# Kernel tuning notes

Measured on AMD Instinct MI355X. Metric: run time of the kernel, lower is better.

The kernel has to match this reference:

```python
import jax, jax.numpy as jnp
import numpy as np
import math

D_MODEL = 1024
NUM_HEADS = 16
D_K = D_MODEL // NUM_HEADS
THETA = 10000.0
NEG_INF = 1.0e6  # module uses -1e6, not -inf


def _rope_tables(seq_len):
    pair_idx = jnp.arange(0, D_K, 2, dtype=jnp.float32)
    inv_freq = 1.0 / (THETA ** (pair_idx / D_K))
    pos = jnp.arange(seq_len, dtype=jnp.float32)
    angles = jnp.outer(pos, inv_freq)  # (S, D_K//2)
    return jnp.cos(angles), jnp.sin(angles)


def _apply_rope(x, cos, sin):
    # x: (B, H, S, D_K); cos/sin: (S, D_K//2)
    xe = x[..., 0::2]
    xo = x[..., 1::2]
    oe = xe * cos - xo * sin
    oo = xe * sin + xo * cos
    return jnp.stack([oe, oo], axis=-1).reshape(x.shape)


def setup_inputs() -> dict:
    key = jax.random.key(0)
    k0, k1, k2, k3, k4 = jax.random.split(key, 5)
    B, S = 2, 2048
    x = jax.random.normal(k0, (B, S, D_MODEL), dtype=jnp.float32)
    scale = 0.02
    wq = jax.random.normal(k1, (D_MODEL, D_MODEL), dtype=jnp.float32) * scale
    wk = jax.random.normal(k2, (D_MODEL, D_MODEL), dtype=jnp.float32) * scale
    wv = jax.random.normal(k3, (D_MODEL, D_MODEL), dtype=jnp.float32) * scale
    wo = jax.random.normal(k4, (D_MODEL, D_MODEL), dtype=jnp.float32) * scale
    return {"x": x, "wq": wq, "wk": wk, "wv": wv, "wo": wo}


def reference(x, wq, wk, wv, wo):
    B, S, _ = x.shape
    q = x @ wq.T
    k = x @ wk.T
    v = x @ wv.T
    # (B, S, H, d_k) -> (B, H, S, d_k)
    q = q.reshape(B, S, NUM_HEADS, D_K).transpose(0, 2, 1, 3)
    k = k.reshape(B, S, NUM_HEADS, D_K).transpose(0, 2, 1, 3)
    v = v.reshape(B, S, NUM_HEADS, D_K).transpose(0, 2, 1, 3)
    cos, sin = _rope_tables(S)
    q = _apply_rope(q, cos, sin)
    k = _apply_rope(k, cos, sin)
    scores = jnp.einsum("bhqd,bhkd->bhqk", q, k) / math.sqrt(D_K)
    causal = jnp.tril(jnp.ones((S, S), dtype=bool))
    scores = jnp.where(causal, scores, -NEG_INF)
    attn = jax.nn.softmax(scores, axis=-1)
    out = jnp.einsum("bhqk,bhkd->bhqd", attn, v)
    out = out.transpose(0, 2, 1, 3).reshape(B, S, D_MODEL)
    return out @ wo.T
```

## Files before the change

### kernel.cpp

```cpp
#include <hip/hip_runtime.h>

typedef __attribute__((ext_vector_type(8))) __bf16 bf16x8;
typedef __attribute__((ext_vector_type(8))) _Float16 f16x8;
typedef __attribute__((ext_vector_type(4))) float f32x4;
typedef __attribute__((ext_vector_type(8))) unsigned short u16x8;
typedef __attribute__((ext_vector_type(4))) unsigned int u32x4;

#define MFMA_BF16(a, b, c) __builtin_amdgcn_mfma_f32_16x16x32_bf16((a), (b), (c), 0, 0, 0)
#define MFMA_F16(a, b, c)  __builtin_amdgcn_mfma_f32_16x16x32_f16((a), (b), (c), 0, 0, 0)
#define LOG2E 1.44269504088896340736f
#define QSCALE 0.18033688011112042f

__device__ __forceinline__ float b2f(unsigned short u) {
    union { unsigned int i; float f; } v; v.i = ((unsigned int)u) << 16; return v.f;
}
__device__ __forceinline__ unsigned short f2bf(float f) {
    union { float f; unsigned int i; } v; v.f = f;
    unsigned int u = v.i;
    return (unsigned short)((u + 0x7fffu + ((u >> 16) & 1u)) >> 16);
}

__device__ __forceinline__ void gl_lds16(const void* g, void* l) {
    __builtin_amdgcn_global_load_lds(
        (const __attribute__((address_space(1))) void*)g,
        (__attribute__((address_space(3))) void*)l,
        16, 0, 0);
}

__global__ __launch_bounds__(256) void cvt_all(const float* __restrict__ x,
                                               const float* __restrict__ wq,
                                               const float* __restrict__ wk,
                                               const float* __restrict__ wv,
                                               const float* __restrict__ wo,
                                               unsigned short* __restrict__ xb,
                                               unsigned short* __restrict__ wqb,
                                               unsigned short* __restrict__ wkb,
                                               unsigned short* __restrict__ wvb,
                                               unsigned short* __restrict__ wob) {
    int id = blockIdx.x * 256 + threadIdx.x;
    const float* src; unsigned short* dst; size_t off; float scl = 1.0f;
    if (id < 524288)      { src = x;  dst = xb;  off = (size_t)id * 8; }
    else if (id < 655360) { src = wq; dst = wqb; off = (size_t)(id - 524288) * 8; scl = QSCALE; }
    else if (id < 786432) { src = wk; dst = wkb; off = (size_t)(id - 655360) * 8; }
    else if (id < 917504) { src = wv; dst = wvb; off = (size_t)(id - 786432) * 8; }
    else                  { src = wo; dst = wob; off = (size_t)(id - 917504) * 8; }
    float4 a = *(const float4*)(src + off);
    float4 b = *(const float4*)(src + off + 4);
    u16x8 o;
    o[0] = f2bf(a.x * scl); o[1] = f2bf(a.y * scl); o[2] = f2bf(a.z * scl); o[3] = f2bf(a.w * scl);
    o[4] = f2bf(b.x * scl); o[5] = f2bf(b.y * scl); o[6] = f2bf(b.z * scl); o[7] = f2bf(b.w * scl);
    *(u16x8*)(dst + off) = o;
}

template <int MODE>
__device__ __forceinline__ void gemm128_bt(const unsigned short* __restrict__ A,
                                           const unsigned short* __restrict__ B,
                                           void* __restrict__ Cv,
                                           int m0, int n0, int ldc,
                                           unsigned short* As, unsigned short* Bs) {
    const int tid = threadIdx.x;
    const int w = tid >> 6, lane = tid & 63;
    const int quad = lane >> 4, l15 = lane & 15;
    const int wm = w & 1, wn = w >> 1;

    f32x4 acc[4][4];
#pragma unroll
    for (int mt = 0; mt < 4; ++mt)
#pragma unroll
        for (int nt = 0; nt < 4; ++nt) acc[mt][nt] = f32x4{0.f, 0.f, 0.f, 0.f};

    for (int k0 = 0; k0 < 1024; k0 += 32) {
        __syncthreads();
#pragma unroll
        for (int i = 0; i < 2; ++i) {
            int L = (w * 2 + i) * 64 + lane;
            int r = L >> 2;
            int c = (L & 3) ^ ((r >> 1) & 3);
            gl_lds16(A + (size_t)(m0 + r) * 1024 + k0 + c * 8, As + L * 8);
            gl_lds16(B + (size_t)(n0 + r) * 1024 + k0 + c * 8, Bs + L * 8);
        }
        __syncthreads();

        bf16x8 af[4], bfr[4];
#pragma unroll
        for (int mt = 0; mt < 4; ++mt) {
            int row = wm * 64 + mt * 16 + l15;
            af[mt] = *(const bf16x8*)(As + row * 32 + (quad ^ ((row >> 1) & 3)) * 8);
        }
#pragma unroll
        for (int nt = 0; nt < 4; ++nt) {
            int row = wn * 64 + nt * 16 + l15;
            bfr[nt] = *(const bf16x8*)(Bs + row * 32 + (quad ^ ((row >> 1) & 3)) * 8);
        }
#pragma unroll
        for (int mt = 0; mt < 4; ++mt)
#pragma unroll
            for (int nt = 0; nt < 4; ++nt)
                acc[mt][nt] = MFMA_BF16(af[mt], bfr[nt], acc[mt][nt]);
    }

    float invf[4], sgn = 0.f;
    if constexpr (MODE == 3) {
        sgn = (l15 & 1) ? 1.0f : -1.0f;
#pragma unroll
        for (int nt = 0; nt < 4; ++nt)
            invf[nt] = exp2f(-0.41524101186092029f * (float)((nt * 16 + l15) >> 1));
    }

#pragma unroll
    for (int mt = 0; mt < 4; ++mt) {
        int grow = m0 + wm * 64 + mt * 16 + quad * 4;
#pragma unroll
        for (int nt = 0; nt < 4; ++nt) {
            int gcol = n0 + wn * 64 + nt * 16 + l15;
#pragma unroll
            for (int r = 0; r < 4; ++r) {
                float val = acc[mt][nt][r];
                size_t idx = (size_t)(grow + r) * ldc + gcol;
                if constexpr (MODE == 0) {
                    ((unsigned short*)Cv)[idx] = f2bf(val);
                } else if constexpr (MODE == 1) {
                    ((float*)Cv)[idx] = val;
                } else if constexpr (MODE == 2) {
                    _Float16 hv = (_Float16)val;
                    ((unsigned short*)Cv)[idx] = __builtin_bit_cast(unsigned short, hv);
                } else {
                    float p = __shfl_xor(val, 1);
                    float pos = (float)((grow + r) & 2047);
                    float ang = pos * invf[nt];
                    float out = val * __cosf(ang) + sgn * p * __sinf(ang);
                    ((unsigned short*)Cv)[idx] = f2bf(out);
                }
            }
        }
    }
}

__global__ __launch_bounds__(256) void gemm_qkv(const unsigned short* __restrict__ X,
                                                const unsigned short* __restrict__ Wq,
                                                const unsigned short* __restrict__ Wk,
                                                const unsigned short* __restrict__ Wv,
                                                unsigned short* __restrict__ Qo,
                                                unsigned short* __restrict__ Ko,
                                                unsigned short* __restrict__ Vt) {
    __shared__ unsigned short As[128 * 32];
    __shared__ unsigned short Bs[128 * 32];
    int y = blockIdx.y;
    if (y < 16) {
        int sel = y >> 3;
        int m0 = blockIdx.x * 128;
        int n0 = (y & 7) * 128;
        const unsigned short* B = sel ? Wk : Wq;
        unsigned short* C = sel ? Ko : Qo;
        gemm128_bt<3>(X, B, C, m0, n0, 1024, As, Bs);
    } else {
        int m0 = (y & 7) * 128;
        int n0 = blockIdx.x * 128;
        gemm128_bt<2>(Wv, X, Vt, m0, n0, 4096, As, Bs);
    }
}

__global__ __launch_bounds__(256) void gemm_out(const unsigned short* __restrict__ A,
                                                const unsigned short* __restrict__ Wo,
                                                float* __restrict__ C) {
    __shared__ unsigned short As[128 * 32];
    __shared__ unsigned short Bs[128 * 32];
    gemm128_bt<1>(A, Wo, C, blockIdx.x * 128, blockIdx.y * 128, 1024, As, Bs);
}

#define FBODY(KBASE, MASKED)                                                            \
    {                                                                                   \
        bf16x8 kf[4][2];                                                                \
        _Pragma("unroll")                                                               \
        for (int nt = 0; nt < 4; ++nt) {                                                \
            int row = nt * 16 + l15;                                                    \
            const unsigned short* kp = Ksb + row * 64;                                  \
            int swk = row & 7;                                                          \
            kf[nt][0] = *(const bf16x8*)(kp + (quad ^ swk) * 8);                        \
            kf[nt][1] = *(const bf16x8*)(kp + ((quad ^ 4) ^ swk) * 8);                  \
        }                                                                               \
        f16x8 pa[2][2];                                                                 \
        _Pragma("unroll")                                                               \
        for (int mt = 0; mt < 2; ++mt) {                                                \
            f32x4 sc[4];                                                                \
            _Pragma("unroll")                                                           \
            for (int nt = 0; nt < 4; ++nt) {                                            \
                f32x4 z = f32x4{0.f, 0.f, 0.f, 0.f};                                    \
                z = MFMA_BF16(kf[nt][0], qf[mt][0], z);                                 \
                sc[nt] = MFMA_BF16(kf[nt][1], qf[mt][1], z);                            \
            }                                                                           \
            int qpos = qposw + mt * 16 + l15;                                           \
            unsigned pk[8];                                                             \
            _Pragma("unroll")                                                           \
            for (int nt = 0; nt < 4; ++nt) {                                            \
                float e[4];                                                             \
                _Pragma("unroll")                                                       \
                for (int r_ = 0; r_ < 4; ++r_) {                                        \
                    float ev = exp2f(sc[nt][r_]);                                       \
                    if (MASKED) {                                                       \
                        int kpos = (KBASE) + nt * 16 + quad * 4 + r_;                   \
                        ev = (kpos > qpos) ? 0.f : ev;                                  \
                    }                                                                   \
                    e[r_] = ev;                                                         \
                }                                                                       \
                pk[nt * 2 + 0] = __builtin_bit_cast(unsigned,                           \
                                     __builtin_amdgcn_cvt_pkrtz(e[0], e[1]));           \
                pk[nt * 2 + 1] = __builtin_bit_cast(unsigned,                           \
                                     __builtin_amdgcn_cvt_pkrtz(e[2], e[3]));           \
            }                                                                           \
            u32x4 rs0 = u32x4{pk[0], pk[1], pk[2], pk[3]};                              \
            u32x4 rs1 = u32x4{pk[4], pk[5], pk[6], pk[7]};                              \
            lacc[mt] = MFMA_F16(__builtin_bit_cast(f16x8, rs0), ones, lacc[mt]);        \
            lacc[mt] = MFMA_F16(__builtin_bit_cast(f16x8, rs1), ones, lacc[mt]);        \
            int b0 = quad & 1;                                                          \
            unsigned y0 = (unsigned)__builtin_amdgcn_ds_swizzle(                        \
                              (int)(b0 ? pk[0] : pk[2]), 0x401F);                       \
            unsigned y1 = (unsigned)__builtin_amdgcn_ds_swizzle(                        \
                              (int)(b0 ? pk[1] : pk[3]), 0x401F);                       \
            unsigned y2 = (unsigned)__builtin_amdgcn_ds_swizzle(                        \
                              (int)(b0 ? pk[4] : pk[6]), 0x401F);                       \
            unsigned y3 = (unsigned)__builtin_amdgcn_ds_swizzle(                        \
                              (int)(b0 ? pk[5] : pk[7]), 0x401F);                       \
            u32x4 t0 = b0 ? u32x4{y0, y1, pk[2], pk[3]}                                 \
                          : u32x4{pk[0], pk[1], y0, y1};                                \
            u32x4 t1 = b0 ? u32x4{y2, y3, pk[6], pk[7]}                                 \
                          : u32x4{pk[4], pk[5], y2, y3};                                \
            pa[mt][0] = __builtin_bit_cast(f16x8, t0);                                  \
            pa[mt][1] = __builtin_bit_cast(f16x8, t1);                                  \
        }                                                                               \
        _Pragma("unroll")                                                               \
        for (int nt = 0; nt < 4; ++nt) {                                                \
            int rowd = nt * 16 + l15;                                                   \
            const unsigned short* vp = Vsb + rowd * 64;                                 \
            int sl0 = pi4 ^ (rowd & 7);                                                 \
            f16x8 v0 = *(const f16x8*)(vp + sl0 * 8);                                   \
            f16x8 v1 = *(const f16x8*)(vp + (sl0 ^ 4) * 8);                             \
            accO[0][nt] = MFMA_F16(pa[0][0], v0, accO[0][nt]);                          \
            accO[1][nt] = MFMA_F16(pa[1][0], v0, accO[1][nt]);                          \
            accO[0][nt] = MFMA_F16(pa[0][1], v1, accO[0][nt]);                          \
            accO[1][nt] = MFMA_F16(pa[1][1], v1, accO[1][nt]);                          \
        }                                                                               \
    }

__global__ __launch_bounds__(512, 4) void flash_attn(const unsigned short* __restrict__ Q,
                                                     const unsigned short* __restrict__ Kb,
                                                     const unsigned short* __restrict__ Vt,
                                                     unsigned short* __restrict__ O) {
    int id = blockIdx.x;
    int xcd = id & 7;
    int s  = id >> 3;
    int rr = s & 3;
    int t  = s >> 2;
    int qt = (t < 8) ? t : 23 - t;
    int bh = xcd + 8 * rr;
    int b = bh >> 4, h = bh & 15;
    int tid = threadIdx.x;
    int wv8 = tid >> 6;
    int g = wv8 >> 2;
    int w = wv8 & 3;
    int lane = tid & 63;
    int quad = lane >> 4, l15 = lane & 15;
    int pi4 = ((quad & 1) << 1) | (quad >> 1);

    __shared__ __align__(16) float Red[10240];
    unsigned short* Ks = (unsigned short*)Red;
    unsigned short* Vs = Ks + 8192;

    int r = tid >> 3, c = (tid & 7) ^ (r & 7);
    const unsigned short* KgT = Kb + (size_t)(b * 2048 + r) * 1024 + h * 64 + c * 8;
    const unsigned short* VgT = Vt + (size_t)(h * 64 + r) * 4096 + b * 2048 + c * 8;

    int qrow0 = b * 2048 + qt * 128 + w * 32;
    int qposw = qt * 128 + w * 32;
    int nit = qt + 1;

    bf16x8 qf[2][2];
#pragma unroll
    for (int mt = 0; mt < 2; ++mt) {
        const unsigned short* qp =
            Q + (size_t)(qrow0 + mt * 16 + l15) * 1024 + h * 64 + quad * 8;
        qf[mt][0] = *(const bf16x8*)qp;
        qf[mt][1] = *(const bf16x8*)(qp + 32);
    }

    f16x8 ones;
#pragma unroll
    for (int tt = 0; tt < 8; ++tt) ones[tt] = (_Float16)1.0f;

    f32x4 accO[2][4];
    f32x4 lacc[2];
#pragma unroll
    for (int mt = 0; mt < 2; ++mt) {
        lacc[mt] = f32x4{0.f, 0.f, 0.f, 0.f};
#pragma unroll
        for (int nt = 0; nt < 4; ++nt) accO[mt][nt] = f32x4{0.f, 0.f, 0.f, 0.f};
    }

    for (int it = 0; it < nit; ++it) {
        __syncthreads();
        {
            size_t ko = (size_t)(it * 128) * 1024;
            int vo = it * 128;
            gl_lds16(KgT + ko, Ks + tid * 8);
            gl_lds16(KgT + ko + 64 * 1024, Ks + 4096 + tid * 8);
            gl_lds16(VgT + vo, Vs + tid * 8);
            gl_lds16(VgT + vo + 64, Vs + 4096 + tid * 8);
        }
        __syncthreads();
        const unsigned short* Ksb = Ks + g * 4096;
        const unsigned short* Vsb = Vs + g * 4096;
        int kbase = it * 128 + g * 64;
        if (it < nit - 1) {
            FBODY(kbase, 0)
        } else {
            FBODY(kbase, 1)
        }
    }

    __syncthreads();
    if (g == 1) {
        float* dst = Red + (w * 64 + lane) * 32;
#pragma unroll
        for (int mt = 0; mt < 2; ++mt)
#pragma unroll
            for (int nt = 0; nt < 4; ++nt)
                *(f32x4*)(dst + mt * 16 + nt * 4) = accO[mt][nt];
        float* dl = Red + 8192 + (w * 64 + lane) * 8;
        *(f32x4*)(dl)     = lacc[0];
        *(f32x4*)(dl + 4) = lacc[1];
    }
    __syncthreads();
    if (g == 0) {
        const float* src = Red + (w * 64 + lane) * 32;
#pragma unroll
        for (int mt = 0; mt < 2; ++mt)
#pragma unroll
            for (int nt = 0; nt < 4; ++nt)
                accO[mt][nt] += *(const f32x4*)(src + mt * 16 + nt * 4);
        const float* dl = Red + 8192 + (w * 64 + lane) * 8;
        lacc[0] += *(const f32x4*)(dl);
        lacc[1] += *(const f32x4*)(dl + 4);

#pragma unroll
        for (int mt = 0; mt < 2; ++mt) {
            float inv[4];
#pragma unroll
            for (int r_ = 0; r_ < 4; ++r_) inv[r_] = 1.0f / lacc[mt][r_];
#pragma unroll
            for (int nt = 0; nt < 4; ++nt)
#pragma unroll
                for (int r_ = 0; r_ < 4; ++r_)
                    O[(size_t)(qrow0 + mt * 16 + quad * 4 + r_) * 1024 +
                      h * 64 + nt * 16 + l15] = f2bf(accO[mt][nt][r_] * inv[r_]);
        }
    }
}

extern "C" void kernel_launch(void* const* d_in, const int* in_sizes, int n_in,
                              void* d_out, int out_size, void* d_ws, size_t ws_size,
                              hipStream_t stream) {
    (void)in_sizes; (void)n_in; (void)out_size; (void)ws_size;
    const float* x  = (const float*)d_in[0];
    const float* wq = (const float*)d_in[1];
    const float* wk = (const float*)d_in[2];
    const float* wv = (const float*)d_in[3];
    const float* wo = (const float*)d_in[4];
    float* out = (float*)d_out;

    const size_t T = (size_t)4096 * 1024;
    const size_t W = (size_t)1024 * 1024;
    unsigned short* Q   = (unsigned short*)d_ws;
    unsigned short* K   = Q + T;
    unsigned short* Vt  = K + T;
    unsigned short* xb  = Vt + T;
    unsigned short* AO  = xb;
    unsigned short* wqb = xb + T;
    unsigned short* wkb = wqb + W;
    unsigned short* wvb = wkb + W;
    unsigned short* wob = wvb + W;

    cvt_all  <<<dim3(4096),   256, 0, stream>>>(x, wq, wk, wv, wo, xb, wqb, wkb, wvb, wob);
    gemm_qkv <<<dim3(32, 24), 256, 0, stream>>>(xb, wqb, wkb, wvb, Q, K, Vt);
    flash_attn<<<dim3(512),   512, 0, stream>>>(Q, K, Vt, AO);
    gemm_out <<<dim3(32, 8),  256, 0, stream>>>(AO, wob, out);
}
```

Measured before the change: 181.4 us.

## Double-buffer K/V tiles in LDS and drop P swizzle via permuted V reads

Converts the flash-attention loop to a two-stage LDS pipeline, prefetching the next K/V tile with async global-to-LDS loads while the current tile is computed, and replacing two barriers per iteration with one. It also removes the ds_swizzle shuffle of the probability fragments by reading V from LDS as four half-width chunks in a matching permuted order, and restrides the final reduction buffer to avoid bank conflicts. In exchange LDS use grows to 64KB per block, which may lower occupancy against the 4-blocks launch bound, and V reads become 8-byte instead of 16-byte loads.

```diff
diff --git a/kernel.cpp b/kernel.cpp
--- a/kernel.cpp
+++ b/kernel.cpp
@@ -2,6 +2,7 @@
 
 typedef __attribute__((ext_vector_type(8))) __bf16 bf16x8;
 typedef __attribute__((ext_vector_type(8))) _Float16 f16x8;
+typedef __attribute__((ext_vector_type(4))) _Float16 f16x4;
 typedef __attribute__((ext_vector_type(4))) float f32x4;
 typedef __attribute__((ext_vector_type(8))) unsigned short u16x8;
 typedef __attribute__((ext_vector_type(4))) unsigned int u32x4;
@@ -208,33 +209,25 @@
                 pk[nt * 2 + 1] = __builtin_bit_cast(unsigned,                           \
                                      __builtin_amdgcn_cvt_pkrtz(e[2], e[3]));           \
             }                                                                           \
-            u32x4 rs0 = u32x4{pk[0], pk[1], pk[2], pk[3]};                              \
-            u32x4 rs1 = u32x4{pk[4], pk[5], pk[6], pk[7]};                              \
-            lacc[mt] = MFMA_F16(__builtin_bit_cast(f16x8, rs0), ones, lacc[mt]);        \
-            lacc[mt] = MFMA_F16(__builtin_bit_cast(f16x8, rs1), ones, lacc[mt]);        \
-            int b0 = quad & 1;                                                          \
-            unsigned y0 = (unsigned)__builtin_amdgcn_ds_swizzle(                        \
-                              (int)(b0 ? pk[0] : pk[2]), 0x401F);                       \
-            unsigned y1 = (unsigned)__builtin_amdgcn_ds_swizzle(                        \
-                              (int)(b0 ? pk[1] : pk[3]), 0x401F);                       \
-            unsigned y2 = (unsigned)__builtin_amdgcn_ds_swizzle(                        \
-                              (int)(b0 ? pk[4] : pk[6]), 0x401F);                       \
-            unsigned y3 = (unsigned)__builtin_amdgcn_ds_swizzle(                        \
-                              (int)(b0 ? pk[5] : pk[7]), 0x401F);                       \
-            u32x4 t0 = b0 ? u32x4{y0, y1, pk[2], pk[3]}                                 \
-                          : u32x4{pk[0], pk[1], y0, y1};                                \
-            u32x4 t1 = b0 ? u32x4{y2, y3, pk[6], pk[7]}                                 \
-                          : u32x4{pk[4], pk[5], y2, y3};                                \
-            pa[mt][0] = __builtin_bit_cast(f16x8, t0);                                  \
-            pa[mt][1] = __builtin_bit_cast(f16x8, t1);                                  \
+            u32x4 w0 = u32x4{pk[0], pk[1], pk[2], pk[3]};                               \
+            u32x4 w1 = u32x4{pk[4], pk[5], pk[6], pk[7]};                               \
+            pa[mt][0] = __builtin_bit_cast(f16x8, w0);                                  \
+            pa[mt][1] = __builtin_bit_cast(f16x8, w1);                                  \
+            lacc[mt] = MFMA_F16(pa[mt][0], ones, lacc[mt]);                             \
+            lacc[mt] = MFMA_F16(pa[mt][1], ones, lacc[mt]);                             \
         }                                                                               \
         _Pragma("unroll")                                                               \
         for (int nt = 0; nt < 4; ++nt) {                                                \
-            int rowd = nt * 16 + l15;                                                   \
-            const unsigned short* vp = Vsb + rowd * 64;                                 \
-            int sl0 = pi4 ^ (rowd & 7);                                                 \
-            f16x8 v0 = *(const f16x8*)(vp + sl0 * 8);                                   \
-            f16x8 v1 = *(const f16x8*)(vp + (sl0 ^ 4) * 8);                             \
+            int row = nt * 16 + l15;                                                    \
+            int sw = row & 7;                                                           \
+            const unsigned short* vp = Vsb + row * 64 + (quad & 1) * 4;                 \
+            int ch = quad >> 1;                                                         \
+            f16x4 a0 = *(const f16x4*)(vp + ((ch + 0) ^ sw) * 8);                       \
+            f16x4 a1 = *(const f16x4*)(vp + ((ch + 2) ^ sw) * 8);                       \
+            f16x4 a2 = *(const f16x4*)(vp + ((ch + 4) ^ sw) * 8);                       \
+            f16x4 a3 = *(const f16x4*)(vp + ((ch + 6) ^ sw) * 8);                       \
+            f16x8 v0 = __builtin_shufflevector(a0, a1, 0, 1, 2, 3, 4, 5, 6, 7);         \
+            f16x8 v1 = __builtin_shufflevector(a2, a3, 0, 1, 2, 3, 4, 5, 6, 7);         \
             accO[0][nt] = MFMA_F16(pa[0][0], v0, accO[0][nt]);                          \
             accO[1][nt] = MFMA_F16(pa[1][0], v0, accO[1][nt]);                          \
             accO[0][nt] = MFMA_F16(pa[0][1], v1, accO[0][nt]);                          \
@@ -260,11 +253,11 @@
     int w = wv8 & 3;
     int lane = tid & 63;
     int quad = lane >> 4, l15 = lane & 15;
-    int pi4 = ((quad & 1) << 1) | (quad >> 1);
-
-    __shared__ __align__(16) float Red[10240];
-    unsigned short* Ks = (unsigned short*)Red;
-    unsigned short* Vs = Ks + 8192;
+
+    __shared__ __align__(16) unsigned short Sh[32768];
+    unsigned short* Ks = Sh;
+    unsigned short* Vs = Sh + 16384;
+    float* Red = (float*)Sh;
 
     int r = tid >> 3, c = (tid & 7) ^ (r & 7);
     const unsigned short* KgT = Kb + (size_t)(b * 2048 + r) * 1024 + h * 64 + c * 8;
@@ -296,50 +289,57 @@
         for (int nt = 0; nt < 4; ++nt) accO[mt][nt] = f32x4{0.f, 0.f, 0.f, 0.f};
     }
 
+#define STAGE(it_, buf_)                                                    \
+    {                                                                       \
+        size_t ko = (size_t)(it_) * 131072;                                 \
+        int vo = (it_) * 128;                                               \
+        unsigned short* kd = Ks + (buf_) * 8192 + tid * 8;                  \
+        unsigned short* vd = Vs + (buf_) * 8192 + tid * 8;                  \
+        gl_lds16(KgT + ko, kd);                                             \
+        gl_lds16(KgT + ko + 65536, kd + 4096);                              \
+        gl_lds16(VgT + vo, vd);                                             \
+        gl_lds16(VgT + vo + 64, vd + 4096);                                 \
+    }
+
+    STAGE(0, 0)
+    __asm__ volatile("s_waitcnt vmcnt(0)" ::: "memory");
+    __builtin_amdgcn_s_barrier();
+
     for (int it = 0; it < nit; ++it) {
-        __syncthreads();
-        {
-            size_t ko = (size_t)(it * 128) * 1024;
-            int vo = it * 128;
-            gl_lds16(KgT + ko, Ks + tid * 8);
-            gl_lds16(KgT + ko + 64 * 1024, Ks + 4096 + tid * 8);
-            gl_lds16(VgT + vo, Vs + tid * 8);
-            gl_lds16(VgT + vo + 64, Vs + 4096 + tid * 8);
-        }
-        __syncthreads();
-        const unsigned short* Ksb = Ks + g * 4096;
-        const unsigned short* Vsb = Vs + g * 4096;
+        if (it + 1 < nit) STAGE(it + 1, (it + 1) & 1)
+        const unsigned short* Ksb = Ks + (it & 1) * 8192 + g * 4096;
+        const unsigned short* Vsb = Vs + (it & 1) * 8192 + g * 4096;
         int kbase = it * 128 + g * 64;
         if (it < nit - 1) {
             FBODY(kbase, 0)
         } else {
             FBODY(kbase, 1)
         }
+        __asm__ volatile("s_waitcnt vmcnt(0) lgkmcnt(0)" ::: "memory");
+        __builtin_amdgcn_s_barrier();
     }
 
     __syncthreads();
     if (g == 1) {
-        float* dst = Red + (w * 64 + lane) * 32;
+        float* dst = Red + (size_t)(w * 64 + lane) * 4;
 #pragma unroll
         for (int mt = 0; mt < 2; ++mt)
 #pragma unroll
             for (int nt = 0; nt < 4; ++nt)
-                *(f32x4*)(dst + mt * 16 + nt * 4) = accO[mt][nt];
-        float* dl = Red + 8192 + (w * 64 + lane) * 8;
-        *(f32x4*)(dl)     = lacc[0];
-        *(f32x4*)(dl + 4) = lacc[1];
+                *(f32x4*)(dst + (mt * 4 + nt) * 1024) = accO[mt][nt];
+        *(f32x4*)(dst + 8 * 1024) = lacc[0];
+        *(f32x4*)(dst + 9 * 1024) = lacc[1];
     }
     __syncthreads();
     if (g == 0) {
-        const float* src = Red + (w * 64 + lane) * 32;
+        const float* src = Red + (size_t)(w * 64 + lane) * 4;
 #pragma unroll
         for (int mt = 0; mt < 2; ++mt)
 #pragma unroll
             for (int nt = 0; nt < 4; ++nt)
-                accO[mt][nt] += *(const f32x4*)(src + mt * 16 + nt * 4);
-        const float* dl = Red + 8192 + (w * 64 + lane) * 8;
-        lacc[0] += *(const f32x4*)(dl);
-        lacc[1] += *(const f32x4*)(dl + 4);
+                accO[mt][nt] += *(const f32x4*)(src + (mt * 4 + nt) * 1024);
+        lacc[0] += *(const f32x4*)(src + 8 * 1024);
+        lacc[1] += *(const f32x4*)(src + 9 * 1024);
 
 #pragma unroll
         for (int mt = 0; mt < 2; ++mt) {
@@ -354,6 +354,7 @@
                       h * 64 + nt * 16 + l15] = f2bf(accO[mt][nt][r_] * inv[r_]);
         }
     }
+#undef STAGE
 }
 
 extern "C" void kernel_launch(void* const* d_in, const int* in_sizes, int n_in,
```

After: 190.3 us. 1.05x slower.
